# Kernel optimization log

Hardware: AMD Instinct MI355X
Metric: run time of the kernel (lower is better)

Reference implementation:

```python
import jax, jax.numpy as jnp
import numpy as np

CARDS = [1000000, 500000, 100000, 50000, 10000, 10000, 5000, 5000, 1000, 1000,
         500, 500, 100, 100, 50, 50, 20, 20, 10, 10, 5, 5, 3, 3, 2, 2]

def _emb_dim(card):
    return int(min(32, max(4, round(1.6 * card ** 0.56))))

DIMS = [_emb_dim(c) for c in CARDS]          # per-table embedding dims (torch rule)
ROWS = [c + 1 for c in CARDS]                # +1 for UNK row at index 0 (padding_idx)
OFFS = np.concatenate([[0], np.cumsum(ROWS)[:-1]]).astype(np.int64)
TOTAL_ROWS = int(sum(ROWS))
MAX_D = 32
NUM_CONT = 64
B = 131072
CAT_DIM = int(sum(DIMS))                     # 508
FUSED_IN = CAT_DIM + 32                      # cont MLP outputs 32
LN_EPS = 1e-5


def setup_inputs() -> dict:
    key = jax.random.key(0)
    ks = jax.random.split(key, 10)
    x_cont = jax.random.normal(ks[0], (B, NUM_CONT), dtype=jnp.float32)
    # per-column indices in [0, card_i] (0 = UNK/padding)
    cols = [jax.random.randint(jax.random.fold_in(ks[1], i), (B,), 0, r, dtype=jnp.int64)
            for i, r in enumerate(ROWS)]
    x_cat = jnp.stack(cols, axis=1)  # [B, 26] int64
    # all tables stacked into one flat [TOTAL_ROWS, 32] array; table i uses cols [:DIMS[i]]
    emb_flat = jax.random.normal(ks[2], (TOTAL_ROWS, MAX_D), dtype=jnp.float32) * 0.05
    emb_flat = emb_flat.at[np.asarray(OFFS)].set(0.0)  # padding_idx=0 rows are zero
    # cont MLP: Linear(64,32) + LayerNorm(32) + SiLU
    Wc = jax.random.normal(ks[3], (NUM_CONT, 32), dtype=jnp.float32) * (1.0 / np.sqrt(NUM_CONT))
    bc = jnp.zeros((32,), jnp.float32)
    ln_g = jnp.ones((32,), jnp.float32)
    ln_b = jnp.zeros((32,), jnp.float32)
    # proj: Linear(540,64)+SiLU, Linear(64,32)+SiLU (dropout = identity in eval)
    W1 = jax.random.normal(ks[4], (FUSED_IN, 64), dtype=jnp.float32) * (1.0 / np.sqrt(FUSED_IN))
    b1 = jnp.zeros((64,), jnp.float32)
    W2 = jax.random.normal(ks[5], (64, 32), dtype=jnp.float32) * (1.0 / np.sqrt(64))
    b2 = jnp.zeros((32,), jnp.float32)
    return {"x_cont": x_cont, "x_cat": x_cat, "emb_flat": emb_flat,
            "Wc": Wc, "bc": bc, "ln_g": ln_g, "ln_b": ln_b,
            "W1": W1, "b1": b1, "W2": W2, "b2": b2}


def reference(x_cont, x_cat, emb_flat, Wc, bc, ln_g, ln_b, W1, b1, W2, b2):
    # --- multi-table embedding gather + concat (eval: dropout = identity) ---
    gidx = x_cat + jnp.asarray(OFFS)[None, :]          # [B, T] global row ids
    rows = emb_flat[gidx]                               # [B, T, 32] single fused gather
    rows = rows * (x_cat != 0).astype(rows.dtype)[..., None]  # padding_idx semantics
    cat = jnp.concatenate([rows[:, i, :d] for i, d in enumerate(DIMS)], axis=1)  # [B, 508]
    # --- cont MLP: Linear + LayerNorm + SiLU ---
    h = x_cont @ Wc + bc                                # [B, 32]
    mu = jnp.mean(h, axis=-1, keepdims=True)
    var = jnp.var(h, axis=-1, keepdims=True)
    h = (h - mu) / jnp.sqrt(var + LN_EPS) * ln_g + ln_b
    h = jax.nn.silu(h)
    # --- fuse + proj MLP ---
    fused = jnp.concatenate([h, cat], axis=1)           # [B, 540]
    z = jax.nn.silu(fused @ W1 + b1)                    # [B, 64]
    z = jax.nn.silu(z @ W2 + b2)                        # [B, 32]
    return z
```

## Files before the change

### kernel.cpp

```cpp
#include <hip/hip_runtime.h>

typedef __attribute__((ext_vector_type(8))) short bf16x8;
typedef __attribute__((ext_vector_type(4))) float f32x4;

#define NT 26
#define BROWS 32
#define NKH 9
#define LDSTR 584
#define Z1STR 68
#define WS_FRAG_DWORDS 18432

__constant__ int4 c_TAB[NT] = {
    {0,32,8,0},{1000001,64,8,0},{1500002,96,8,0},{1600003,128,8,0},
    {1650004,160,8,0},{1660005,192,8,0},{1670006,224,8,0},{1675007,256,8,0},
    {1680008,288,8,0},{1681009,320,8,0},{1682010,352,8,0},{1682511,384,8,0},
    {1683012,416,6,0},{1683113,440,6,0},{1683214,464,4,0},{1683265,480,4,0},
    {1683316,496,3,0},{1683337,508,3,0},{1683358,520,2,0},{1683369,528,2,0},
    {1683380,536,1,0},{1683386,540,1,0},{1683392,544,1,0},{1683396,548,1,0},
    {1683400,552,1,0},{1683403,556,1,0}};

__constant__ int c_P_COLP[NT] = {
    0,32,64,96,128,160,192,224,256,288,320,352,384,408,432,448,464,476,
    488,496,504,508,512,516,520,524};
__constant__ int c_P_DIMS[NT] = {
    32,32,32,32,32,32,32,32,32,32,32,32,21,21,14,14,9,9,6,6,4,4,4,4,4,4};
__constant__ int c_P_COLF[NT] = {
    0,32,64,96,128,160,192,224,256,288,320,352,384,405,426,440,454,463,
    472,478,484,488,492,496,500,504};

__device__ __forceinline__ unsigned short f2bf(float f) {
  unsigned int u = __builtin_bit_cast(unsigned int, f);
  u += 0x7fffu + ((u >> 16) & 1u);
  return (unsigned short)(u >> 16);
}

__device__ __forceinline__ unsigned cvtpk(float a, float b) {
  unsigned r;
  asm("v_cvt_pk_bf16_f32 %0, %1, %2" : "=v"(r) : "v"(a), "v"(b));
  return r;
}

__device__ __forceinline__ float silu_f(float x) {
  return x / (1.0f + __expf(-x));
}

extern "C" __global__ void __launch_bounds__(256)
prep_w1(const float* __restrict__ W1, unsigned int* __restrict__ wsf) {
  const int g = blockIdx.x * 256 + threadIdx.x;
  if (g >= WS_FRAG_DWORDS) return;
  const int f  = g * 2;
  const int j  = f & 7;
  const int l  = (f >> 3) & 63;
  const int w  = (f >> 9) & 3;
  const int ks = f >> 11;
  const int bn = (w << 4) + (l & 15);
  const int k0 = (ks << 5) + ((l >> 4) << 3) + j;
  float v[2];
  #pragma unroll
  for (int e = 0; e < 2; ++e) {
    const int k = k0 + e;
    float x = 0.0f;
    if (k < 32) {
      x = W1[k * 64 + bn];
    } else {
      const int c = k - 32;
      for (int i = 0; i < NT; ++i) {
        const int off = c - c_P_COLP[i];
        if (off >= 0 && off < c_P_DIMS[i])
          x = W1[(32 + c_P_COLF[i] + off) * 64 + bn];
      }
    }
    v[e] = x;
  }
  wsf[g] = ((unsigned)f2bf(v[0])) | (((unsigned)f2bf(v[1])) << 16);
}

__device__ __forceinline__ void gather_one(const float* __restrict__ emb,
                                           unsigned short* __restrict__ fused,
                                           int p, int idx) {
  const int i = p >> 5;
  const int r = p & 31;
  const int4 tb = c_TAB[i];
  const float4* src = (const float4*)(emb + (size_t)(tb.x + idx) * 32);
  char* dstb = (char*)fused + r * (LDSTR * 2) + tb.y * 2;
  if (tb.z == 8) {
    const float4 f0 = src[0], f1 = src[1], f2 = src[2], f3 = src[3];
    const float4 f4 = src[4], f5 = src[5], f6 = src[6], f7 = src[7];
    uint4 o0, o1, o2, o3;
    o0.x = cvtpk(f0.x, f0.y); o0.y = cvtpk(f0.z, f0.w);
    o0.z = cvtpk(f1.x, f1.y); o0.w = cvtpk(f1.z, f1.w);
    o1.x = cvtpk(f2.x, f2.y); o1.y = cvtpk(f2.z, f2.w);
    o1.z = cvtpk(f3.x, f3.y); o1.w = cvtpk(f3.z, f3.w);
    o2.x = cvtpk(f4.x, f4.y); o2.y = cvtpk(f4.z, f4.w);
    o2.z = cvtpk(f5.x, f5.y); o2.w = cvtpk(f5.z, f5.w);
    o3.x = cvtpk(f6.x, f6.y); o3.y = cvtpk(f6.z, f6.w);
    o3.z = cvtpk(f7.x, f7.y); o3.w = cvtpk(f7.z, f7.w);
    uint4* d4 = (uint4*)dstb;
    d4[0] = o0; d4[1] = o1; d4[2] = o2; d4[3] = o3;
  } else {
    uint2* d2 = (uint2*)dstb;
    for (int c4 = 0; c4 < tb.z; ++c4) {
      const float4 fv = src[c4];
      uint2 o;
      o.x = cvtpk(fv.x, fv.y);
      o.y = cvtpk(fv.z, fv.w);
      d2[c4] = o;
    }
  }
}

extern "C" __global__ void __launch_bounds__(256, 2)
tab_fused(const float* __restrict__ xc,
          const int* __restrict__ xcat,
          const float* __restrict__ emb,
          const float* __restrict__ Wc,
          const float* __restrict__ bc,
          const float* __restrict__ lng,
          const float* __restrict__ lnb,
          const unsigned short* __restrict__ wsf,
          const float* __restrict__ b1,
          const float* __restrict__ W2,
          const float* __restrict__ b2,
          float* __restrict__ out) {
  __shared__ __attribute__((aligned(16))) float smem[(BROWS * LDSTR) / 2];
  unsigned short* fused = (unsigned short*)smem;
  float* z1 = smem;

  const int t  = threadIdx.x;
  const int w  = t >> 6;
  const int l  = t & 63;
  const int R0 = blockIdx.x * BROWS;

  const int bn = (w << 4) + (l & 15);
  const int kg = (l >> 4) << 3;

  bf16x8 bfw[NKH];
  #pragma unroll
  for (int ks = 0; ks < NKH; ++ks)
    bfw[ks] = *(const bf16x8*)(wsf + (((ks) * 4 + w) * 64 + l) * 8);
  if (t < 64) {
    uint4 zz = {0u, 0u, 0u, 0u};
    *(uint4*)((char*)fused + (t >> 1) * (LDSTR * 2) + (560 + (t & 1) * 8) * 2) = zz;
  }

  int pidx[4];
  #pragma unroll
  for (int it = 0; it < 3; ++it) {
    const int p = t + it * 256;
    pidx[it] = xcat[(size_t)(R0 + (p & 31)) * NT + (p >> 5)];
  }
  if (t < 64) pidx[3] = xcat[(size_t)(R0 + (t & 31)) * NT + ((t + 768) >> 5)];
  #pragma unroll
  for (int it = 0; it < 3; ++it) gather_one(emb, fused, t + it * 256, pidx[it]);
  if (t < 64) gather_one(emb, fused, t + 768, pidx[3]);

  {
    const int r  = t >> 3;
    const int j0 = (t & 7) << 2;
    const float* xr = xc + (size_t)(R0 + r) * 64;
    float h0 = bc[j0], h1 = bc[j0 + 1], h2 = bc[j0 + 2], h3 = bc[j0 + 3];
    #pragma unroll 4
    for (int k4 = 0; k4 < 16; ++k4) {
      const float4 x4 = ((const float4*)xr)[k4];
      const float* wb = Wc + (k4 * 4) * 32 + j0;
      const float4 w0 = *(const float4*)(wb);
      const float4 w1 = *(const float4*)(wb + 32);
      const float4 w2 = *(const float4*)(wb + 64);
      const float4 w3 = *(const float4*)(wb + 96);
      h0 = __fmaf_rn(x4.x, w0.x, h0); h1 = __fmaf_rn(x4.x, w0.y, h1);
      h2 = __fmaf_rn(x4.x, w0.z, h2); h3 = __fmaf_rn(x4.x, w0.w, h3);
      h0 = __fmaf_rn(x4.y, w1.x, h0); h1 = __fmaf_rn(x4.y, w1.y, h1);
      h2 = __fmaf_rn(x4.y, w1.z, h2); h3 = __fmaf_rn(x4.y, w1.w, h3);
      h0 = __fmaf_rn(x4.z, w2.x, h0); h1 = __fmaf_rn(x4.z, w2.y, h1);
      h2 = __fmaf_rn(x4.z, w2.z, h2); h3 = __fmaf_rn(x4.z, w2.w, h3);
      h0 = __fmaf_rn(x4.w, w3.x, h0); h1 = __fmaf_rn(x4.w, w3.y, h1);
      h2 = __fmaf_rn(x4.w, w3.z, h2); h3 = __fmaf_rn(x4.w, w3.w, h3);
    }
    float s1 = h0 + h1 + h2 + h3;
    float s2 = h0 * h0 + h1 * h1 + h2 * h2 + h3 * h3;
    #pragma unroll
    for (int m = 1; m < 8; m <<= 1) {
      s1 += __shfl_xor(s1, m);
      s2 += __shfl_xor(s2, m);
    }
    const float mu = s1 * 0.03125f;
    const float var = s2 * 0.03125f - mu * mu;
    const float rs = rsqrtf(var + 1e-5f);
    const float g0 = silu_f((h0 - mu) * rs * lng[j0]     + lnb[j0]);
    const float g1 = silu_f((h1 - mu) * rs * lng[j0 + 1] + lnb[j0 + 1]);
    const float g2 = silu_f((h2 - mu) * rs * lng[j0 + 2] + lnb[j0 + 2]);
    const float g3 = silu_f((h3 - mu) * rs * lng[j0 + 3] + lnb[j0 + 3]);
    uint2 hw;
    hw.x = cvtpk(g0, g1);
    hw.y = cvtpk(g2, g3);
    *(uint2*)((char*)fused + r * (LDSTR * 2) + j0 * 2) = hw;
  }
  __syncthreads();

  f32x4 acc[2];
  acc[0] = (f32x4){0.f, 0.f, 0.f, 0.f};
  acc[1] = (f32x4){0.f, 0.f, 0.f, 0.f};
  const unsigned short* arow0 = &fused[(l & 15) * LDSTR + kg];
  const unsigned short* arow1 = arow0 + 16 * LDSTR;
  #pragma unroll
  for (int ks = 0; ks < NKH; ++ks) {
    acc[0] = __builtin_amdgcn_mfma_f32_16x16x32_bf16(
        *(const bf16x8*)(arow0 + (ks << 5)), bfw[ks], acc[0], 0, 0, 0);
    acc[1] = __builtin_amdgcn_mfma_f32_16x16x32_bf16(
        *(const bf16x8*)(arow1 + (ks << 5)), bfw[ks], acc[1], 0, 0, 0);
  }
  #pragma unroll
  for (int ks = 0; ks < NKH; ++ks)
    bfw[ks] = *(const bf16x8*)(wsf + (((NKH + ks) * 4 + w) * 64 + l) * 8);
  #pragma unroll
  for (int ks = 0; ks < NKH; ++ks) {
    acc[0] = __builtin_amdgcn_mfma_f32_16x16x32_bf16(
        *(const bf16x8*)(arow0 + 288 + (ks << 5)), bfw[ks], acc[0], 0, 0, 0);
    acc[1] = __builtin_amdgcn_mfma_f32_16x16x32_bf16(
        *(const bf16x8*)(arow1 + 288 + (ks << 5)), bfw[ks], acc[1], 0, 0, 0);
  }
  __syncthreads();

  {
    const float b1v = b1[bn];
    const int rb = (l >> 4) << 2;
    #pragma unroll
    for (int mt = 0; mt < 2; ++mt) {
      #pragma unroll
      for (int v = 0; v < 4; ++v) {
        const int row = (mt << 4) + rb + v;
        z1[row * Z1STR + bn] = silu_f(acc[mt][v] + b1v);
      }
    }
  }
  __syncthreads();

  {
    const int r  = t >> 3;
    const int j0 = (t & 7) << 2;
    float a0 = b2[j0], a1 = b2[j0 + 1], a2 = b2[j0 + 2], a3 = b2[j0 + 3];
    const float* zr = &z1[r * Z1STR];
    #pragma unroll 8
    for (int k = 0; k < 64; ++k) {
      const float zv = zr[k];
      const float4 w2v = *(const float4*)(W2 + k * 32 + j0);
      a0 = __fmaf_rn(zv, w2v.x, a0);
      a1 = __fmaf_rn(zv, w2v.y, a1);
      a2 = __fmaf_rn(zv, w2v.z, a2);
      a3 = __fmaf_rn(zv, w2v.w, a3);
    }
    float4 o;
    o.x = silu_f(a0); o.y = silu_f(a1); o.z = silu_f(a2); o.w = silu_f(a3);
    *(float4*)(out + (size_t)(R0 + r) * 32 + j0) = o;
  }
}

extern "C" void kernel_launch(void* const* d_in, const int* in_sizes, int n_in,
                              void* d_out, int out_size, void* d_ws, size_t ws_size,
                              hipStream_t stream) {
  const float* xc   = (const float*)d_in[0];
  const int*   xcat = (const int*)  d_in[1];
  const float* emb  = (const float*)d_in[2];
  const float* Wc   = (const float*)d_in[3];
  const float* bc   = (const float*)d_in[4];
  const float* lng  = (const float*)d_in[5];
  const float* lnb  = (const float*)d_in[6];
  const float* W1   = (const float*)d_in[7];
  const float* b1   = (const float*)d_in[8];
  const float* W2   = (const float*)d_in[9];
  const float* b2   = (const float*)d_in[10];
  float* out = (float*)d_out;

  unsigned int* wsf = (unsigned int*)d_ws;
  hipLaunchKernelGGL(prep_w1, dim3((WS_FRAG_DWORDS + 255) / 256), dim3(256),
                     0, stream, W1, wsf);

  const int B = in_sizes[0] / 64;
  const int grid = B / BROWS;
  hipLaunchKernelGGL(tab_fused, dim3(grid), dim3(256), 0, stream,
                     xc, xcat, emb, Wc, bc, lng, lnb,
                     (const unsigned short*)wsf, b1, W2, b2, out);
}
```

Before: 126.9 us.

## Issue all embedding loads up front and load full W1 fragments before MFMA

Changes the gather so each thread statically owns table slots: tables i, i+8 and i+16, plus one of 24/25 for the first 64 threads. All embedding row loads are issued together before any LDS writes, which removes the per-slot branching and serialized load-convert-store chains. All 18 W1 fragment slices are loaded into registers once, after the cont MLP, instead of in two halves, so the second-half load no longer stalls between MFMA groups. The W2 layer is also vectorised with float4 reads from LDS. The trade-off is much higher register pressure (18 bf16x8 fragments plus many float4 loads), which could hurt occupancy under the 2-blocks-per-SM launch bound.

```diff
diff --git a/kernel.cpp b/kernel.cpp
--- a/kernel.cpp
+++ b/kernel.cpp
@@ -5,7 +5,7 @@
 
 #define NT 26
 #define BROWS 32
-#define NKH 9
+#define NKS 18
 #define LDSTR 584
 #define Z1STR 68
 #define WS_FRAG_DWORDS 18432
@@ -38,6 +38,19 @@
   unsigned r;
   asm("v_cvt_pk_bf16_f32 %0, %1, %2" : "=v"(r) : "v"(a), "v"(b));
   return r;
+}
+
+__device__ __forceinline__ uint4 pk4(float4 a, float4 b) {
+  uint4 o;
+  o.x = cvtpk(a.x, a.y); o.y = cvtpk(a.z, a.w);
+  o.z = cvtpk(b.x, b.y); o.w = cvtpk(b.z, b.w);
+  return o;
+}
+
+__device__ __forceinline__ uint2 pk2(float4 a) {
+  uint2 o;
+  o.x = cvtpk(a.x, a.y); o.y = cvtpk(a.z, a.w);
+  return o;
 }
 
 __device__ __forceinline__ float silu_f(float x) {
@@ -75,40 +88,6 @@
   wsf[g] = ((unsigned)f2bf(v[0])) | (((unsigned)f2bf(v[1])) << 16);
 }
 
-__device__ __forceinline__ void gather_one(const float* __restrict__ emb,
-                                           unsigned short* __restrict__ fused,
-                                           int p, int idx) {
-  const int i = p >> 5;
-  const int r = p & 31;
-  const int4 tb = c_TAB[i];
-  const float4* src = (const float4*)(emb + (size_t)(tb.x + idx) * 32);
-  char* dstb = (char*)fused + r * (LDSTR * 2) + tb.y * 2;
-  if (tb.z == 8) {
-    const float4 f0 = src[0], f1 = src[1], f2 = src[2], f3 = src[3];
-    const float4 f4 = src[4], f5 = src[5], f6 = src[6], f7 = src[7];
-    uint4 o0, o1, o2, o3;
-    o0.x = cvtpk(f0.x, f0.y); o0.y = cvtpk(f0.z, f0.w);
-    o0.z = cvtpk(f1.x, f1.y); o0.w = cvtpk(f1.z, f1.w);
-    o1.x = cvtpk(f2.x, f2.y); o1.y = cvtpk(f2.z, f2.w);
-    o1.z = cvtpk(f3.x, f3.y); o1.w = cvtpk(f3.z, f3.w);
-    o2.x = cvtpk(f4.x, f4.y); o2.y = cvtpk(f4.z, f4.w);
-    o2.z = cvtpk(f5.x, f5.y); o2.w = cvtpk(f5.z, f5.w);
-    o3.x = cvtpk(f6.x, f6.y); o3.y = cvtpk(f6.z, f6.w);
-    o3.z = cvtpk(f7.x, f7.y); o3.w = cvtpk(f7.z, f7.w);
-    uint4* d4 = (uint4*)dstb;
-    d4[0] = o0; d4[1] = o1; d4[2] = o2; d4[3] = o3;
-  } else {
-    uint2* d2 = (uint2*)dstb;
-    for (int c4 = 0; c4 < tb.z; ++c4) {
-      const float4 fv = src[c4];
-      uint2 o;
-      o.x = cvtpk(fv.x, fv.y);
-      o.y = cvtpk(fv.z, fv.w);
-      d2[c4] = o;
-    }
-  }
-}
-
 extern "C" __global__ void __launch_bounds__(256, 2)
 tab_fused(const float* __restrict__ xc,
           const int* __restrict__ xcat,
@@ -134,25 +113,61 @@
   const int bn = (w << 4) + (l & 15);
   const int kg = (l >> 4) << 3;
 
-  bf16x8 bfw[NKH];
-  #pragma unroll
-  for (int ks = 0; ks < NKH; ++ks)
-    bfw[ks] = *(const bf16x8*)(wsf + (((ks) * 4 + w) * 64 + l) * 8);
+  const int r_ = t & 31;
+  const int i0 = t >> 5;
+  const bool has3 = (t < 64);
+  const int i3 = 24 + (t >> 5);
+  const int* xrow = xcat + (size_t)(R0 + r_) * NT;
+  const int idx0 = xrow[i0];
+  const int idx1 = xrow[i0 + 8];
+  const int idx2 = xrow[i0 + 16];
+  const int idx3 = has3 ? xrow[i3] : 0;
+
+  const int4 tb0 = c_TAB[i0];
+  const int4 tb1 = c_TAB[i0 + 8];
+  const int4 tb2 = c_TAB[i0 + 16];
+  const int4 tb3 = c_TAB[has3 ? i3 : 24];
+
+  const float4* s0 = (const float4*)(emb + (size_t)(tb0.x + idx0) * 32);
+  const float4* s1 = (const float4*)(emb + (size_t)(tb1.x + idx1) * 32);
+  const float4* s2 = (const float4*)(emb + (size_t)(tb2.x + idx2) * 32);
+  const float4* s3 = (const float4*)(emb + (size_t)(tb3.x + idx3) * 32);
+
+  const float4 A0 = s0[0], A1 = s0[1], A2 = s0[2], A3 = s0[3];
+  const float4 A4 = s0[4], A5 = s0[5], A6 = s0[6], A7 = s0[7];
+  const float4 B0 = s1[0], B1 = s1[1], B2 = s1[2], B3 = s1[3];
+  const float4 B4 = s1[4], B5 = s1[5], B6 = s1[6], B7 = s1[7];
+  const float4 C0 = s2[0], C1 = s2[1], C2 = s2[2];
+  float4 D0;
+  if (has3) D0 = s3[0];
+
   if (t < 64) {
     uint4 zz = {0u, 0u, 0u, 0u};
     *(uint4*)((char*)fused + (t >> 1) * (LDSTR * 2) + (560 + (t & 1) * 8) * 2) = zz;
   }
 
-  int pidx[4];
-  #pragma unroll
-  for (int it = 0; it < 3; ++it) {
-    const int p = t + it * 256;
-    pidx[it] = xcat[(size_t)(R0 + (p & 31)) * NT + (p >> 5)];
-  }
-  if (t < 64) pidx[3] = xcat[(size_t)(R0 + (t & 31)) * NT + ((t + 768) >> 5)];
-  #pragma unroll
-  for (int it = 0; it < 3; ++it) gather_one(emb, fused, t + it * 256, pidx[it]);
-  if (t < 64) gather_one(emb, fused, t + 768, pidx[3]);
+  char* rowb = (char*)fused + r_ * (LDSTR * 2);
+  {
+    uint4* d4 = (uint4*)(rowb + tb0.y * 2);
+    d4[0] = pk4(A0, A1); d4[1] = pk4(A2, A3);
+    d4[2] = pk4(A4, A5); d4[3] = pk4(A6, A7);
+  }
+  {
+    uint4* d4 = (uint4*)(rowb + tb1.y * 2);
+    d4[0] = pk4(B0, B1); d4[1] = pk4(B2, B3);
+    if (tb1.z >= 6) d4[2] = pk4(B4, B5);
+    if (tb1.z == 8) d4[3] = pk4(B6, B7);
+  }
+  {
+    uint2* d2 = (uint2*)(rowb + tb2.y * 2);
+    d2[0] = pk2(C0);
+    if (tb2.z >= 2) d2[1] = pk2(C1);
+    if (tb2.z == 3) d2[2] = pk2(C2);
+  }
+  if (has3) {
+    uint2* d2 = (uint2*)(rowb + tb3.y * 2);
+    d2[0] = pk2(D0);
+  }
 
   {
     const int r  = t >> 3;
@@ -176,15 +191,15 @@
       h0 = __fmaf_rn(x4.w, w3.x, h0); h1 = __fmaf_rn(x4.w, w3.y, h1);
       h2 = __fmaf_rn(x4.w, w3.z, h2); h3 = __fmaf_rn(x4.w, w3.w, h3);
     }
-    float s1 = h0 + h1 + h2 + h3;
-    float s2 = h0 * h0 + h1 * h1 + h2 * h2 + h3 * h3;
+    float s1v = h0 + h1 + h2 + h3;
+    float s2v = h0 * h0 + h1 * h1 + h2 * h2 + h3 * h3;
     #pragma unroll
     for (int m = 1; m < 8; m <<= 1) {
-      s1 += __shfl_xor(s1, m);
-      s2 += __shfl_xor(s2, m);
-    }
-    const float mu = s1 * 0.03125f;
-    const float var = s2 * 0.03125f - mu * mu;
+      s1v += __shfl_xor(s1v, m);
+      s2v += __shfl_xor(s2v, m);
+    }
+    const float mu = s1v * 0.03125f;
+    const float var = s2v * 0.03125f - mu * mu;
     const float rs = rsqrtf(var + 1e-5f);
     const float g0 = silu_f((h0 - mu) * rs * lng[j0]     + lnb[j0]);
     const float g1 = silu_f((h1 - mu) * rs * lng[j0 + 1] + lnb[j0 + 1]);
@@ -195,6 +210,11 @@
     hw.y = cvtpk(g2, g3);
     *(uint2*)((char*)fused + r * (LDSTR * 2) + j0 * 2) = hw;
   }
+
+  bf16x8 bfw[NKS];
+  #pragma unroll
+  for (int ks = 0; ks < NKS; ++ks)
+    bfw[ks] = *(const bf16x8*)(wsf + ((ks * 4 + w) * 64 + l) * 8);
   __syncthreads();
 
   f32x4 acc[2];
@@ -203,21 +223,11 @@
   const unsigned short* arow0 = &fused[(l & 15) * LDSTR + kg];
   const unsigned short* arow1 = arow0 + 16 * LDSTR;
   #pragma unroll
-  for (int ks = 0; ks < NKH; ++ks) {
+  for (int ks = 0; ks < NKS; ++ks) {
     acc[0] = __builtin_amdgcn_mfma_f32_16x16x32_bf16(
         *(const bf16x8*)(arow0 + (ks << 5)), bfw[ks], acc[0], 0, 0, 0);
     acc[1] = __builtin_amdgcn_mfma_f32_16x16x32_bf16(
         *(const bf16x8*)(arow1 + (ks << 5)), bfw[ks], acc[1], 0, 0, 0);
-  }
-  #pragma unroll
-  for (int ks = 0; ks < NKH; ++ks)
-    bfw[ks] = *(const bf16x8*)(wsf + (((NKH + ks) * 4 + w) * 64 + l) * 8);
-  #pragma unroll
-  for (int ks = 0; ks < NKH; ++ks) {
-    acc[0] = __builtin_amdgcn_mfma_f32_16x16x32_bf16(
-        *(const bf16x8*)(arow0 + 288 + (ks << 5)), bfw[ks], acc[0], 0, 0, 0);
-    acc[1] = __builtin_amdgcn_mfma_f32_16x16x32_bf16(
-        *(const bf16x8*)(arow1 + 288 + (ks << 5)), bfw[ks], acc[1], 0, 0, 0);
   }
   __syncthreads();
 
@@ -239,15 +249,23 @@
     const int r  = t >> 3;
     const int j0 = (t & 7) << 2;
     float a0 = b2[j0], a1 = b2[j0 + 1], a2 = b2[j0 + 2], a3 = b2[j0 + 3];
-    const float* zr = &z1[r * Z1STR];
-    #pragma unroll 8
-    for (int k = 0; k < 64; ++k) {
-      const float zv = zr[k];
-      const float4 w2v = *(const float4*)(W2 + k * 32 + j0);
-      a0 = __fmaf_rn(zv, w2v.x, a0);
-      a1 = __fmaf_rn(zv, w2v.y, a1);
-      a2 = __fmaf_rn(zv, w2v.z, a2);
-      a3 = __fmaf_rn(zv, w2v.w, a3);
+    const float4* zr4 = (const float4*)&z1[r * Z1STR];
+    #pragma unroll
+    for (int k4 = 0; k4 < 16; ++k4) {
+      const float4 zv = zr4[k4];
+      const float* w2b = W2 + (k4 * 4) * 32 + j0;
+      const float4 w0 = *(const float4*)(w2b);
+      const float4 w1 = *(const float4*)(w2b + 32);
+      const float4 w2v = *(const float4*)(w2b + 64);
+      const float4 w3 = *(const float4*)(w2b + 96);
+      a0 = __fmaf_rn(zv.x, w0.x, a0); a1 = __fmaf_rn(zv.x, w0.y, a1);
+      a2 = __fmaf_rn(zv.x, w0.z, a2); a3 = __fmaf_rn(zv.x, w0.w, a3);
+      a0 = __fmaf_rn(zv.y, w1.x, a0); a1 = __fmaf_rn(zv.y, w1.y, a1);
+      a2 = __fmaf_rn(zv.y, w1.z, a2); a3 = __fmaf_rn(zv.y, w1.w, a3);
+      a0 = __fmaf_rn(zv.z, w2v.x, a0); a1 = __fmaf_rn(zv.z, w2v.y, a1);
+      a2 = __fmaf_rn(zv.z, w2v.z, a2); a3 = __fmaf_rn(zv.z, w2v.w, a3);
+      a0 = __fmaf_rn(zv.w, w3.x, a0); a1 = __fmaf_rn(zv.w, w3.y, a1);
+      a2 = __fmaf_rn(zv.w, w3.z, a2); a3 = __fmaf_rn(zv.w, w3.w, a3);
     }
     float4 o;
     o.x = silu_f(a0); o.y = silu_f(a1); o.z = silu_f(a2); o.w = silu_f(a3);
```

New measurement: 125.9 us. Within noise of the previous version (-0.8%).

## Gather embeddings directly into LDS with async loads and shrink block to eight rows

Applied to the files above, without the earlier changes.

Replaces register-staged embedding gather and bf16 packing with global_load_lds 16-byte async copies into an XOR-swizzled fp32 LDS layout, converting to bf16 at MFMA operand load time. Block rows drop from 32 to 8, giving more, smaller blocks with higher occupancy (launch bounds 8), and the MFMA uses a single 16-row tile where only 8 rows are valid. This cuts register pressure and gather latency exposure, but wastes half the MFMA work, reloads the W1 fragments per block from global, and relies on a constant lookup table for the swizzle mapping.

```diff
diff --git a/kernel.cpp b/kernel.cpp
--- a/kernel.cpp
+++ b/kernel.cpp
@@ -4,20 +4,45 @@
 typedef __attribute__((ext_vector_type(4))) float f32x4;
 
 #define NT 26
-#define BROWS 32
-#define NKH 9
-#define LDSTR 584
+#define BROWS 8
+#define NKS 18
+#define NGI 17
+#define GBYTES (NGI * 1024)
+#define HF_F (GBYTES / 4)
+#define HSTR 36
+#define ZOFF_F (HF_F + BROWS * HSTR)
+#define SMEM_F (ZOFF_F + 16)
 #define Z1STR 68
 #define WS_FRAG_DWORDS 18432
 
-__constant__ int4 c_TAB[NT] = {
-    {0,32,8,0},{1000001,64,8,0},{1500002,96,8,0},{1600003,128,8,0},
-    {1650004,160,8,0},{1660005,192,8,0},{1670006,224,8,0},{1675007,256,8,0},
-    {1680008,288,8,0},{1681009,320,8,0},{1682010,352,8,0},{1682511,384,8,0},
-    {1683012,416,6,0},{1683113,440,6,0},{1683214,464,4,0},{1683265,480,4,0},
-    {1683316,496,3,0},{1683337,508,3,0},{1683358,520,2,0},{1683369,528,2,0},
-    {1683380,536,1,0},{1683386,540,1,0},{1683392,544,1,0},{1683396,548,1,0},
-    {1683400,552,1,0},{1683403,556,1,0}};
+__constant__ int c_OFFS[NT] = {
+    0,1000001,1500002,1600003,1650004,1660005,1670006,1675007,1680008,1681009,
+    1682010,1682511,1683012,1683113,1683214,1683265,1683316,1683337,1683358,
+    1683369,1683380,1683386,1683392,1683396,1683400,1683403};
+
+__constant__ unsigned short c_QT[136] = {
+  0,256,512,768,1024,1280,1536,1792,
+  1,257,513,769,1025,1281,1537,1793,
+  2,258,514,770,1026,1282,1538,1794,
+  3,259,515,771,1027,1283,1539,1795,
+  4,260,516,772,1028,1284,1540,1796,
+  5,261,517,773,1029,1285,1541,1797,
+  6,262,518,774,1030,1286,1542,1798,
+  7,263,519,775,1031,1287,1543,1799,
+  8,264,520,776,1032,1288,1544,1800,
+  9,265,521,777,1033,1289,1545,1801,
+  10,266,522,778,1034,1290,1546,1802,
+  11,267,523,779,1035,1291,1547,1803,
+  12,268,524,780,1036,1292,
+  13,269,525,781,1037,1293,
+  14,270,526,782,
+  15,271,527,783,
+  16,272,528,
+  17,273,529,
+  18,274,
+  19,275,
+  20,21,22,23,24,25,
+  0,0,0,0};
 
 __constant__ int c_P_COLP[NT] = {
     0,32,64,96,128,160,192,224,256,288,320,352,384,408,432,448,464,476,
@@ -75,41 +100,7 @@
   wsf[g] = ((unsigned)f2bf(v[0])) | (((unsigned)f2bf(v[1])) << 16);
 }
 
-__device__ __forceinline__ void gather_one(const float* __restrict__ emb,
-                                           unsigned short* __restrict__ fused,
-                                           int p, int idx) {
-  const int i = p >> 5;
-  const int r = p & 31;
-  const int4 tb = c_TAB[i];
-  const float4* src = (const float4*)(emb + (size_t)(tb.x + idx) * 32);
-  char* dstb = (char*)fused + r * (LDSTR * 2) + tb.y * 2;
-  if (tb.z == 8) {
-    const float4 f0 = src[0], f1 = src[1], f2 = src[2], f3 = src[3];
-    const float4 f4 = src[4], f5 = src[5], f6 = src[6], f7 = src[7];
-    uint4 o0, o1, o2, o3;
-    o0.x = cvtpk(f0.x, f0.y); o0.y = cvtpk(f0.z, f0.w);
-    o0.z = cvtpk(f1.x, f1.y); o0.w = cvtpk(f1.z, f1.w);
-    o1.x = cvtpk(f2.x, f2.y); o1.y = cvtpk(f2.z, f2.w);
-    o1.z = cvtpk(f3.x, f3.y); o1.w = cvtpk(f3.z, f3.w);
-    o2.x = cvtpk(f4.x, f4.y); o2.y = cvtpk(f4.z, f4.w);
-    o2.z = cvtpk(f5.x, f5.y); o2.w = cvtpk(f5.z, f5.w);
-    o3.x = cvtpk(f6.x, f6.y); o3.y = cvtpk(f6.z, f6.w);
-    o3.z = cvtpk(f7.x, f7.y); o3.w = cvtpk(f7.z, f7.w);
-    uint4* d4 = (uint4*)dstb;
-    d4[0] = o0; d4[1] = o1; d4[2] = o2; d4[3] = o3;
-  } else {
-    uint2* d2 = (uint2*)dstb;
-    for (int c4 = 0; c4 < tb.z; ++c4) {
-      const float4 fv = src[c4];
-      uint2 o;
-      o.x = cvtpk(fv.x, fv.y);
-      o.y = cvtpk(fv.z, fv.w);
-      d2[c4] = o;
-    }
-  }
-}
-
-extern "C" __global__ void __launch_bounds__(256, 2)
+extern "C" __global__ void __launch_bounds__(256, 8)
 tab_fused(const float* __restrict__ xc,
           const int* __restrict__ xcat,
           const float* __restrict__ emb,
@@ -122,9 +113,7 @@
           const float* __restrict__ W2,
           const float* __restrict__ b2,
           float* __restrict__ out) {
-  __shared__ __attribute__((aligned(16))) float smem[(BROWS * LDSTR) / 2];
-  unsigned short* fused = (unsigned short*)smem;
-  float* z1 = smem;
+  __shared__ __attribute__((aligned(16))) float smem[SMEM_F];
 
   const int t  = threadIdx.x;
   const int w  = t >> 6;
@@ -134,124 +123,108 @@
   const int bn = (w << 4) + (l & 15);
   const int kg = (l >> 4) << 3;
 
-  bf16x8 bfw[NKH];
-  #pragma unroll
-  for (int ks = 0; ks < NKH; ++ks)
-    bfw[ks] = *(const bf16x8*)(wsf + (((ks) * 4 + w) * 64 + l) * 8);
-  if (t < 64) {
-    uint4 zz = {0u, 0u, 0u, 0u};
-    *(uint4*)((char*)fused + (t >> 1) * (LDSTR * 2) + (560 + (t & 1) * 8) * 2) = zz;
-  }
-
-  int pidx[4];
-  #pragma unroll
-  for (int it = 0; it < 3; ++it) {
-    const int p = t + it * 256;
-    pidx[it] = xcat[(size_t)(R0 + (p & 31)) * NT + (p >> 5)];
-  }
-  if (t < 64) pidx[3] = xcat[(size_t)(R0 + (t & 31)) * NT + ((t + 768) >> 5)];
-  #pragma unroll
-  for (int it = 0; it < 3; ++it) gather_one(emb, fused, t + it * 256, pidx[it]);
-  if (t < 64) gather_one(emb, fused, t + 768, pidx[3]);
-
-  {
-    const int r  = t >> 3;
-    const int j0 = (t & 7) << 2;
+  {
+    const int row  = l >> 3;
+    const int slot = l & 7;
+    const int qsw  = slot ^ row;
+    #pragma unroll
+    for (int g = 0; g < NGI; ++g) {
+      if ((g & 3) == w) {
+        const unsigned qt = c_QT[g * 8 + qsw];
+        const int tab = qt & 255, q = qt >> 8;
+        const int idx = xcat[(size_t)(R0 + row) * NT + tab];
+        const float* src = emb + ((size_t)(c_OFFS[tab] + idx) << 5) + (q << 2);
+        __builtin_amdgcn_global_load_lds(
+            (const __attribute__((address_space(1))) void*)src,
+            (__attribute__((address_space(3))) void*)((char*)smem + g * 1024),
+            16, 0, 0);
+      }
+    }
+  }
+
+  if (t < 16) smem[ZOFF_F + t] = 0.0f;
+
+  {
+    const int r = t >> 5, j = t & 31;
     const float* xr = xc + (size_t)(R0 + r) * 64;
-    float h0 = bc[j0], h1 = bc[j0 + 1], h2 = bc[j0 + 2], h3 = bc[j0 + 3];
+    float h = bc[j];
     #pragma unroll 4
     for (int k4 = 0; k4 < 16; ++k4) {
       const float4 x4 = ((const float4*)xr)[k4];
-      const float* wb = Wc + (k4 * 4) * 32 + j0;
-      const float4 w0 = *(const float4*)(wb);
-      const float4 w1 = *(const float4*)(wb + 32);
-      const float4 w2 = *(const float4*)(wb + 64);
-      const float4 w3 = *(const float4*)(wb + 96);
-      h0 = __fmaf_rn(x4.x, w0.x, h0); h1 = __fmaf_rn(x4.x, w0.y, h1);
-      h2 = __fmaf_rn(x4.x, w0.z, h2); h3 = __fmaf_rn(x4.x, w0.w, h3);
-      h0 = __fmaf_rn(x4.y, w1.x, h0); h1 = __fmaf_rn(x4.y, w1.y, h1);
-      h2 = __fmaf_rn(x4.y, w1.z, h2); h3 = __fmaf_rn(x4.y, w1.w, h3);
-      h0 = __fmaf_rn(x4.z, w2.x, h0); h1 = __fmaf_rn(x4.z, w2.y, h1);
-      h2 = __fmaf_rn(x4.z, w2.z, h2); h3 = __fmaf_rn(x4.z, w2.w, h3);
-      h0 = __fmaf_rn(x4.w, w3.x, h0); h1 = __fmaf_rn(x4.w, w3.y, h1);
-      h2 = __fmaf_rn(x4.w, w3.z, h2); h3 = __fmaf_rn(x4.w, w3.w, h3);
-    }
-    float s1 = h0 + h1 + h2 + h3;
-    float s2 = h0 * h0 + h1 * h1 + h2 * h2 + h3 * h3;
-    #pragma unroll
-    for (int m = 1; m < 8; m <<= 1) {
+      const float* wb = Wc + (k4 * 4) * 32 + j;
+      h = __fmaf_rn(x4.x, wb[0],  h);
+      h = __fmaf_rn(x4.y, wb[32], h);
+      h = __fmaf_rn(x4.z, wb[64], h);
+      h = __fmaf_rn(x4.w, wb[96], h);
+    }
+    float s1 = h, s2 = h * h;
+    #pragma unroll
+    for (int m = 1; m < 32; m <<= 1) {
       s1 += __shfl_xor(s1, m);
       s2 += __shfl_xor(s2, m);
     }
     const float mu = s1 * 0.03125f;
     const float var = s2 * 0.03125f - mu * mu;
     const float rs = rsqrtf(var + 1e-5f);
-    const float g0 = silu_f((h0 - mu) * rs * lng[j0]     + lnb[j0]);
-    const float g1 = silu_f((h1 - mu) * rs * lng[j0 + 1] + lnb[j0 + 1]);
-    const float g2 = silu_f((h2 - mu) * rs * lng[j0 + 2] + lnb[j0 + 2]);
-    const float g3 = silu_f((h3 - mu) * rs * lng[j0 + 3] + lnb[j0 + 3]);
-    uint2 hw;
-    hw.x = cvtpk(g0, g1);
-    hw.y = cvtpk(g2, g3);
-    *(uint2*)((char*)fused + r * (LDSTR * 2) + j0 * 2) = hw;
+    smem[HF_F + r * HSTR + j] = silu_f((h - mu) * rs * lng[j] + lnb[j]);
   }
   __syncthreads();
 
-  f32x4 acc[2];
-  acc[0] = (f32x4){0.f, 0.f, 0.f, 0.f};
-  acc[1] = (f32x4){0.f, 0.f, 0.f, 0.f};
-  const unsigned short* arow0 = &fused[(l & 15) * LDSTR + kg];
-  const unsigned short* arow1 = arow0 + 16 * LDSTR;
-  #pragma unroll
-  for (int ks = 0; ks < NKH; ++ks) {
-    acc[0] = __builtin_amdgcn_mfma_f32_16x16x32_bf16(
-        *(const bf16x8*)(arow0 + (ks << 5)), bfw[ks], acc[0], 0, 0, 0);
-    acc[1] = __builtin_amdgcn_mfma_f32_16x16x32_bf16(
-        *(const bf16x8*)(arow1 + (ks << 5)), bfw[ks], acc[1], 0, 0, 0);
-  }
-  #pragma unroll
-  for (int ks = 0; ks < NKH; ++ks)
-    bfw[ks] = *(const bf16x8*)(wsf + (((NKH + ks) * 4 + w) * 64 + l) * 8);
-  #pragma unroll
-  for (int ks = 0; ks < NKH; ++ks) {
-    acc[0] = __builtin_amdgcn_mfma_f32_16x16x32_bf16(
-        *(const bf16x8*)(arow0 + 288 + (ks << 5)), bfw[ks], acc[0], 0, 0, 0);
-    acc[1] = __builtin_amdgcn_mfma_f32_16x16x32_bf16(
-        *(const bf16x8*)(arow1 + 288 + (ks << 5)), bfw[ks], acc[1], 0, 0, 0);
+  f32x4 acc = (f32x4){0.f, 0.f, 0.f, 0.f};
+  {
+    const int rowA = l & 7;
+    const char* a1 = (const char*)smem + rowA * 128 + ((kg >> 2) ^ rowA) * 16;
+    const char* a2 = (const char*)smem + rowA * 128 + (((kg >> 2) ^ rowA) ^ 1) * 16;
+    const float* hrow = smem + HF_F + rowA * HSTR + kg;
+    const char* zb = (const char*)(smem + ZOFF_F);
+    #pragma unroll
+    for (int ks = 0; ks < NKS; ++ks) {
+      const bf16x8 bw = *(const bf16x8*)(wsf + ((ks * 4 + w) * 64 + l) * 8);
+      f32x4 lo, hi;
+      if (ks == 0) {
+        lo = *(const f32x4*)hrow;
+        hi = *(const f32x4*)(hrow + 4);
+      } else if (ks == NKS - 1) {
+        const char* p1 = (kg >= 16) ? zb        : (a1 + (NKS - 2) * 1024);
+        const char* p2 = (kg >= 16) ? (zb + 16) : (a2 + (NKS - 2) * 1024);
+        lo = *(const f32x4*)p1;
+        hi = *(const f32x4*)p2;
+      } else {
+        lo = *(const f32x4*)(a1 + (ks - 1) * 1024);
+        hi = *(const f32x4*)(a2 + (ks - 1) * 1024);
+      }
+      uint4 u;
+      u.x = cvtpk(lo.x, lo.y); u.y = cvtpk(lo.z, lo.w);
+      u.z = cvtpk(hi.x, hi.y); u.w = cvtpk(hi.z, hi.w);
+      const bf16x8 a = __builtin_bit_cast(bf16x8, u);
+      acc = __builtin_amdgcn_mfma_f32_16x16x32_bf16(a, bw, acc, 0, 0, 0);
+    }
   }
   __syncthreads();
 
-  {
+  if (l < 32) {
     const float b1v = b1[bn];
     const int rb = (l >> 4) << 2;
     #pragma unroll
-    for (int mt = 0; mt < 2; ++mt) {
-      #pragma unroll
-      for (int v = 0; v < 4; ++v) {
-        const int row = (mt << 4) + rb + v;
-        z1[row * Z1STR + bn] = silu_f(acc[mt][v] + b1v);
-      }
-    }
+    for (int v = 0; v < 4; ++v)
+      smem[(rb + v) * Z1STR + bn] = silu_f(acc[v] + b1v);
   }
   __syncthreads();
 
   {
-    const int r  = t >> 3;
-    const int j0 = (t & 7) << 2;
-    float a0 = b2[j0], a1 = b2[j0 + 1], a2 = b2[j0 + 2], a3 = b2[j0 + 3];
-    const float* zr = &z1[r * Z1STR];
-    #pragma unroll 8
-    for (int k = 0; k < 64; ++k) {
-      const float zv = zr[k];
-      const float4 w2v = *(const float4*)(W2 + k * 32 + j0);
-      a0 = __fmaf_rn(zv, w2v.x, a0);
-      a1 = __fmaf_rn(zv, w2v.y, a1);
-      a2 = __fmaf_rn(zv, w2v.z, a2);
-      a3 = __fmaf_rn(zv, w2v.w, a3);
-    }
-    float4 o;
-    o.x = silu_f(a0); o.y = silu_f(a1); o.z = silu_f(a2); o.w = silu_f(a3);
-    *(float4*)(out + (size_t)(R0 + r) * 32 + j0) = o;
+    const int r = t >> 5, j = t & 31;
+    float a = b2[j];
+    const float4* zr4 = (const float4*)(smem + r * Z1STR);
+    #pragma unroll 4
+    for (int k4 = 0; k4 < 16; ++k4) {
+      const float4 zv = zr4[k4];
+      const float* w2b = W2 + (k4 * 4) * 32 + j;
+      a = __fmaf_rn(zv.x, w2b[0],  a);
+      a = __fmaf_rn(zv.y, w2b[32], a);
+      a = __fmaf_rn(zv.z, w2b[64], a);
+      a = __fmaf_rn(zv.w, w2b[96], a);
+    }
+    out[(size_t)(R0 + r) * 32 + j] = silu_f(a);
   }
 }
 
```

Measured after the change: 158.2 us. +24.7%, slower.
